# Optimization experiments

Hardware: AMD Instinct MI355X
Metric: run time of the kernel (lower is better)

## Reference

```python
import jax, jax.numpy as jnp
import numpy as np

N, E, F_IN, HID, H1, H2, H3, OUT = 10000, 160000, 50, 350, 4, 4, 6, 121


def _gat(x, src, dst, n, W, a_s, a_d, b, heads, C, concat):
    # PyG GATConv (dropout=0, eval): h = xW^T reshaped to [N,H,C]
    h = (x @ W.T).reshape(n, heads, C)
    alpha_src = jnp.einsum('nhc,hc->nh', h, a_s)  # [N,H]
    alpha_dst = jnp.einsum('nhc,hc->nh', h, a_d)  # [N,H]
    e = jax.nn.leaky_relu(alpha_src[src] + alpha_dst[dst], 0.2)  # [E,H]
    # numerically-stable segment softmax over incoming edges of each dst node
    m = jax.ops.segment_max(e, dst, num_segments=n)
    ee = jnp.exp(e - m[dst])
    s = jax.ops.segment_sum(ee, dst, num_segments=n)
    alpha = ee / s[dst]  # self-loops guarantee s > 0
    out = jax.ops.segment_sum(h[src] * alpha[:, :, None], dst, num_segments=n)  # [N,H,C]
    out = out.reshape(n, heads * C) if concat else out.mean(axis=1)
    return out + b


def setup_inputs() -> dict:
    key = jax.random.key(0)
    ks = jax.random.split(key, 16)
    sc = 0.05
    inp = {
        'x': jax.random.normal(ks[0], (N, F_IN), dtype=jnp.float32),
        'edge_index': jax.random.randint(ks[1], (2, E), 0, N, dtype=jnp.int64) if jax.config.jax_enable_x64 else jax.random.randint(ks[1], (2, E), 0, N, dtype=jnp.int32),
        'W1': jax.random.normal(ks[2], (H1 * HID, F_IN), dtype=jnp.float32) * sc,
        'a1s': jax.random.normal(ks[3], (H1, HID), dtype=jnp.float32) * sc,
        'a1d': jax.random.normal(ks[4], (H1, HID), dtype=jnp.float32) * sc,
        'b1': jnp.zeros((H1 * HID,), dtype=jnp.float32),
        'W2': jax.random.normal(ks[5], (H2 * HID, H1 * HID), dtype=jnp.float32) * sc,
        'a2s': jax.random.normal(ks[6], (H2, HID), dtype=jnp.float32) * sc,
        'a2d': jax.random.normal(ks[7], (H2, HID), dtype=jnp.float32) * sc,
        'b2': jnp.zeros((H2 * HID,), dtype=jnp.float32),
        'Wskip': jax.random.normal(ks[8], (H2 * HID, H1 * HID), dtype=jnp.float32) * sc,
        'W3': jax.random.normal(ks[9], (H3 * OUT, H2 * HID), dtype=jnp.float32) * sc,
        'a3s': jax.random.normal(ks[10], (H3, OUT), dtype=jnp.float32) * sc,
        'a3d': jax.random.normal(ks[11], (H3, OUT), dtype=jnp.float32) * sc,
        'b3': jnp.zeros((OUT,), dtype=jnp.float32),
    }
    return inp


def reference(x, edge_index, W1, a1s, a1d, b1, W2, a2s, a2d, b2, Wskip, W3, a3s, a3d, b3):
    n = x.shape[0]
    loops = jnp.arange(n, dtype=edge_index.dtype)  # PyG add_self_loops=True
    src = jnp.concatenate([edge_index[0], loops])
    dst = jnp.concatenate([edge_index[1], loops])
    h = jax.nn.elu(_gat(x, src, dst, n, W1, a1s, a1d, b1, H1, HID, True))
    x_in = h
    h = jax.nn.elu(_gat(h, src, dst, n, W2, a2s, a2d, b2, H2, HID, True))
    h = h + x_in @ Wskip.T  # skip connection (bias=False)
    return _gat(h, src, dst, n, W3, a3s, a3d, b3, H3, OUT, False)
```

## Files before the change

kernel.cpp:

```cpp
#include <hip/hip_runtime.h>
#include <math.h>

#define NNODES 10000
#define NEDGES 160000
#define E2 (NEDGES + NNODES)
#define F_IN 50
#define HIDC 350
#define NH1 4
#define NH2 4
#define NH3 6
#define OUTC 121
#define MAXE 96
#define KP1 64
#define KP2 1408
#define LD3 736
#define ROWSLACK 128

typedef __attribute__((ext_vector_type(8))) short short8;
typedef __attribute__((ext_vector_type(8))) unsigned short ushort8v;
typedef __attribute__((ext_vector_type(4))) float floatx4;

static __device__ __forceinline__ unsigned short f2bf(float f) {
    unsigned u = __float_as_uint(f);
    unsigned r = (u + 0x7fffu + ((u >> 16) & 1u)) >> 16;
    return (unsigned short)r;
}
static __device__ __forceinline__ float bf2f(unsigned short s) {
    return __uint_as_float(((unsigned)s) << 16);
}

#define GLL16(gp, lp)                                                      \
    __builtin_amdgcn_global_load_lds(                                      \
        (const __attribute__((address_space(1))) void*)(gp),               \
        (__attribute__((address_space(3))) void*)(lp), 16, 0, 0)

__global__ void count_kernel(const int* __restrict__ ei, int* __restrict__ cnt) {
    int i = blockIdx.x * blockDim.x + threadIdx.x;
    if (i >= E2) return;
    int dst = (i < NEDGES) ? ei[NEDGES + i] : (i - NEDGES);
    atomicAdd(&cnt[dst], 1);
}

__global__ void scan_kernel(const int* __restrict__ cnt, int* __restrict__ indptr,
                            int* __restrict__ cursor) {
    __shared__ int part[1024];
    int tid = threadIdx.x;
    const int CH = (NNODES + 1023) / 1024;
    int base = tid * CH;
    int s = 0;
    for (int i = 0; i < CH; i++) {
        int idx = base + i;
        if (idx < NNODES) s += cnt[idx];
    }
    part[tid] = s;
    __syncthreads();
    for (int off = 1; off < 1024; off <<= 1) {
        int v = (tid >= off) ? part[tid - off] : 0;
        __syncthreads();
        part[tid] += v;
        __syncthreads();
    }
    int run = (tid == 0) ? 0 : part[tid - 1];
    for (int i = 0; i < CH; i++) {
        int idx = base + i;
        if (idx < NNODES) {
            indptr[idx] = run;
            cursor[idx] = run;
            run += cnt[idx];
        }
    }
    if (tid == 0) indptr[NNODES] = part[1023];
}

__global__ void scatter_kernel(const int* __restrict__ ei, int* __restrict__ cursor,
                               int* __restrict__ esrc) {
    int i = blockIdx.x * blockDim.x + threadIdx.x;
    if (i >= E2) return;
    int src, dst;
    if (i < NEDGES) {
        src = ei[i];
        dst = ei[NEDGES + i];
    } else {
        src = dst = i - NEDGES;
    }
    int pos = atomicAdd(&cursor[dst], 1);
    esrc[pos] = src;
}

__global__ void splitW1_kernel(const float* __restrict__ W1,
                               unsigned short* __restrict__ w1Hi,
                               unsigned short* __restrict__ w1Lo) {
    int k = threadIdx.x;
    int r = blockIdx.x;
    float v = (k < F_IN) ? W1[(size_t)r * F_IN + k] : 0.f;
    unsigned short h = f2bf(v);
    w1Hi[(size_t)r * KP1 + k] = h;
    w1Lo[(size_t)r * KP1 + k] = f2bf(v - bf2f(h));
}

__global__ void splitB_kernel(const float* __restrict__ W2, const float* __restrict__ Wsk,
                              const float* __restrict__ W3,
                              unsigned short* __restrict__ w2Hi,
                              unsigned short* __restrict__ w3Hi) {
    int k = blockIdx.x * blockDim.x + threadIdx.x;
    if (k >= KP2) return;
    int r = blockIdx.y;
    const int K = 1400;
    const float* src;
    unsigned short* hi;
    int row;
    if (r < 1400) { src = W2; row = r; hi = w2Hi; }
    else if (r < 2800) { src = Wsk; row = r - 1400; hi = w2Hi + (size_t)1400 * KP2; }
    else { src = W3; row = r - 2800; hi = w3Hi; }
    float v = (k < K) ? src[(size_t)row * K + k] : 0.f;
    hi[(size_t)row * KP2 + k] = f2bf(v);
}

__global__ void atil_kernel(const float* __restrict__ W, const float* __restrict__ av_s,
                            const float* __restrict__ av_d, float* __restrict__ outS,
                            float* __restrict__ outD, int C, int K, int cchunk) {
    int k = blockIdx.x * 64 + (threadIdx.x & 63);
    if (k >= K) return;
    int h = blockIdx.y;
    int c0 = blockIdx.z * cchunk;
    int c1 = c0 + cchunk;
    if (c1 > C) c1 = C;
    float ss = 0.f, dd = 0.f;
    for (int c = c0; c < c1; c++) {
        float wv = W[((size_t)h * C + c) * K + k];
        ss = fmaf(wv, av_s[h * C + c], ss);
        dd = fmaf(wv, av_d[h * C + c], dd);
    }
    atomicAdd(&outS[(size_t)h * K + k], ss);
    atomicAdd(&outD[(size_t)h * K + k], dd);
}

__global__ void splitAT2_kernel(const float* __restrict__ atall,
                                unsigned short* __restrict__ atHi,
                                unsigned short* __restrict__ atLo) {
    int k = blockIdx.x * 64 + threadIdx.x;
    int r = blockIdx.y;
    float v = 0.f;
    if (k < 1400) {
        if (r < 4) v = atall[400 + r * 1400 + k];
        else if (r < 8) v = atall[6000 + (r - 4) * 1400 + k];
    }
    unsigned short h = f2bf(v);
    atHi[(size_t)r * KP2 + k] = h;
    atLo[(size_t)r * KP2 + k] = f2bf(v - bf2f(h));
}

__global__ __launch_bounds__(256) void alpha1x_kernel(const float* __restrict__ x,
                                                      const float* __restrict__ at1s,
                                                      const float* __restrict__ at1d,
                                                      float* __restrict__ as1,
                                                      float* __restrict__ ad1) {
    int wave = threadIdx.x >> 6, lane = threadIdx.x & 63;
    int n = blockIdx.x * 4 + wave;
    if (n >= NNODES) return;
    int kk = lane < F_IN ? lane : F_IN - 1;
    float v = (lane < F_IN) ? x[(size_t)n * F_IN + lane] : 0.f;
    float p[8];
#pragma unroll
    for (int h = 0; h < 4; h++) {
        p[h] = v * at1s[h * F_IN + kk];
        p[4 + h] = v * at1d[h * F_IN + kk];
    }
#pragma unroll
    for (int s = 0; s < 8; s++)
#pragma unroll
        for (int o = 32; o > 0; o >>= 1) p[s] += __shfl_xor(p[s], o, 64);
    if (lane == 0) {
#pragma unroll
        for (int h = 0; h < 4; h++) {
            as1[n * 4 + h] = p[h];
            ad1[n * 4 + h] = p[4 + h];
        }
    }
}

__global__ void zeropad_kernel(unsigned short* __restrict__ hi) {
    int i = blockIdx.x * 256 + threadIdx.x;
    if (i >= NNODES * 8) return;
    int n = i >> 3, c = 1400 + (i & 7);
    hi[(size_t)n * KP2 + c] = 0;
}

__global__ __launch_bounds__(256) void agg_x(
    const float* __restrict__ x, const float* __restrict__ as_n,
    const float* __restrict__ ad_n, const int* __restrict__ indptr,
    const int* __restrict__ esrc, unsigned short* __restrict__ xaggHi,
    unsigned short* __restrict__ xaggLo) {
    int n = blockIdx.x, tid = threadIdx.x;
    int s = indptr[n], e = indptr[n + 1];
    int deg = e - s;
    if (deg > MAXE) deg = MAXE;
    __shared__ int srcs[MAXE];
    __shared__ float wgt[MAXE * 4];

    if (tid < 64) {
        int lane = tid;
        float adv[4], mx[4], sm[4];
#pragma unroll
        for (int h = 0; h < 4; h++) {
            adv[h] = ad_n[n * 4 + h];
            mx[h] = -1e30f;
            sm[h] = 0.f;
        }
        for (int j = lane; j < deg; j += 64) {
            int sr = esrc[s + j];
            srcs[j] = sr;
#pragma unroll
            for (int h = 0; h < 4; h++) {
                float ev = as_n[sr * 4 + h] + adv[h];
                ev = ev > 0.f ? ev : 0.2f * ev;
                wgt[j * 4 + h] = ev;
                mx[h] = fmaxf(mx[h], ev);
            }
        }
#pragma unroll
        for (int h = 0; h < 4; h++)
#pragma unroll
            for (int o = 32; o > 0; o >>= 1) mx[h] = fmaxf(mx[h], __shfl_xor(mx[h], o, 64));
        for (int j = lane; j < deg; j += 64) {
#pragma unroll
            for (int h = 0; h < 4; h++) {
                float p = __expf(wgt[j * 4 + h] - mx[h]);
                wgt[j * 4 + h] = p;
                sm[h] += p;
            }
        }
#pragma unroll
        for (int h = 0; h < 4; h++) {
#pragma unroll
            for (int o = 32; o > 0; o >>= 1) sm[h] += __shfl_xor(sm[h], o, 64);
            sm[h] = 1.f / sm[h];
        }
        for (int j = lane; j < deg; j += 64) {
#pragma unroll
            for (int h = 0; h < 4; h++) wgt[j * 4 + h] *= sm[h];
        }
    }
    __syncthreads();

    int h = tid >> 6, k = tid & 63;
    float a = 0.f;
    if (k < F_IN) {
        float a2 = 0.f;
        int j = 0;
        for (; j + 1 < deg; j += 2) {
            a = fmaf(wgt[j * 4 + h], x[(size_t)srcs[j] * F_IN + k], a);
            a2 = fmaf(wgt[(j + 1) * 4 + h], x[(size_t)srcs[j + 1] * F_IN + k], a2);
        }
        if (j < deg) a = fmaf(wgt[j * 4 + h], x[(size_t)srcs[j] * F_IN + k], a);
        a += a2;
    }
    unsigned short hi = f2bf(a);
    xaggHi[(size_t)n * 256 + tid] = hi;
    xaggLo[(size_t)n * 256 + tid] = f2bf(a - bf2f(hi));
}

__global__ __launch_bounds__(256, 2) void gemm_h1(
    const unsigned short* __restrict__ xaggHi, const unsigned short* __restrict__ xaggLo,
    const unsigned short* __restrict__ w1Hi, const unsigned short* __restrict__ w1Lo,
    const float* __restrict__ bias, unsigned short* __restrict__ actHi) {
    __shared__ __align__(16) unsigned short sA[2][128 * 32];
    __shared__ __align__(16) unsigned short sB[2][256 * 32];
    int tid = threadIdx.x;
    int wave = tid >> 6, lane = tid & 63;
    int wm = (wave >> 1) * 64, wn = (wave & 1) * 128;
    int fr = lane & 15, kq = lane >> 4;
    int row0 = blockIdx.y * 128, col0 = blockIdx.x * 256;
    int hd = blockIdx.z;

    floatx4 acc[4][8];
#pragma unroll
    for (int i = 0; i < 4; i++)
#pragma unroll
        for (int j = 0; j < 8; j++)
#pragma unroll
            for (int q = 0; q < 4; q++) acc[i][j][q] = 0.f;

    int gpos = lane & 3;
    int rl = lane >> 2;
    int gsw = kq ^ ((fr >> 1) & 3);

    for (int k0 = 0; k0 < 64; k0 += 32) {
#pragma unroll
        for (int c = 0; c < 2; ++c) {
            int r = wave * 32 + c * 16 + rl;
            int g = gpos ^ ((r >> 1) & 3);
            size_t gofs = (size_t)(row0 + r) * 256 + hd * 64 + k0 + g * 8;
            size_t lofs = (size_t)r * 32 + (size_t)gpos * 8;
            GLL16(xaggHi + gofs, &sA[0][lofs]);
            GLL16(xaggLo + gofs, &sA[1][lofs]);
        }
#pragma unroll
        for (int c = 0; c < 4; ++c) {
            int r = wave * 64 + c * 16 + rl;
            int g = gpos ^ ((r >> 1) & 3);
            size_t gofs = (size_t)(hd * 350 + col0 + r) * KP1 + k0 + g * 8;
            size_t lofs = (size_t)r * 32 + (size_t)gpos * 8;
            GLL16(w1Hi + gofs, &sB[0][lofs]);
            GLL16(w1Lo + gofs, &sB[1][lofs]);
        }
        __syncthreads();

        short8 ah[4], al[4], bh[8], bl[8];
#pragma unroll
        for (int j = 0; j < 8; j++) {
            int rb = wn + j * 16 + fr;
            bh[j] = *(const short8*)&sB[0][rb * 32 + gsw * 8];
            bl[j] = *(const short8*)&sB[1][rb * 32 + gsw * 8];
        }
#pragma unroll
        for (int i = 0; i < 4; i++) {
            int ra = wm + i * 16 + fr;
            ah[i] = *(const short8*)&sA[0][ra * 32 + gsw * 8];
            al[i] = *(const short8*)&sA[1][ra * 32 + gsw * 8];
        }
#pragma unroll
        for (int i = 0; i < 4; i++)
#pragma unroll
            for (int j = 0; j < 8; j++) {
                acc[i][j] = __builtin_amdgcn_mfma_f32_16x16x32_bf16(ah[i], bh[j],
                                                                   acc[i][j], 0, 0, 0);
                acc[i][j] = __builtin_amdgcn_mfma_f32_16x16x32_bf16(al[i], bh[j],
                                                                   acc[i][j], 0, 0, 0);
                acc[i][j] = __builtin_amdgcn_mfma_f32_16x16x32_bf16(ah[i], bl[j],
                                                                   acc[i][j], 0, 0, 0);
            }
        __syncthreads();
    }

#pragma unroll
    for (int i = 0; i < 4; i++) {
#pragma unroll
        for (int rg = 0; rg < 4; rg++) {
            int rr = row0 + wm + i * 16 + kq * 4 + rg;
            if (rr >= NNODES) continue;
#pragma unroll
            for (int j = 0; j < 8; j++) {
                int cc = col0 + wn + j * 16 + fr;
                if (cc < 350) {
                    int gc = hd * 350 + cc;
                    float v = acc[i][j][rg] + bias[gc];
                    v = v > 0.f ? v : expm1f(v);
                    actHi[(size_t)rr * KP2 + gc] = f2bf(v);
                }
            }
        }
    }
}

__global__ __launch_bounds__(256) void alpha_mfma(
    const unsigned short* __restrict__ act, const unsigned short* __restrict__ tHi,
    const unsigned short* __restrict__ tLo, int H, float* __restrict__ asx,
    float* __restrict__ adx) {
    int wave = threadIdx.x >> 6, lane = threadIdx.x & 63;
    int row0 = (blockIdx.x * 4 + wave) * 16;
    if (row0 >= NNODES) return;
    int fr = lane & 15, kq = lane >> 4;
    floatx4 acc = {0.f, 0.f, 0.f, 0.f};
    const unsigned short* arow = act + (size_t)(row0 + fr) * KP2 + kq * 8;
    const unsigned short* brh = tHi + (size_t)fr * KP2 + kq * 8;
    const unsigned short* brl = tLo + (size_t)fr * KP2 + kq * 8;
#pragma unroll 4
    for (int k0 = 0; k0 < KP2; k0 += 32) {
        short8 a = *(const short8*)(arow + k0);
        short8 vh = *(const short8*)(brh + k0);
        short8 vl = *(const short8*)(brl + k0);
        acc = __builtin_amdgcn_mfma_f32_16x16x32_bf16(a, vh, acc, 0, 0, 0);
        acc = __builtin_amdgcn_mfma_f32_16x16x32_bf16(a, vl, acc, 0, 0, 0);
    }
#pragma unroll
    for (int rg = 0; rg < 4; rg++) {
        int rr = row0 + kq * 4 + rg;
        if (fr < H) asx[rr * H + fr] = acc[rg];
        else if (fr < 2 * H) adx[rr * H + (fr - H)] = acc[rg];
    }
}

template <int H>
__global__ __launch_bounds__(64) void alpha_edge(
    const float* __restrict__ as_n, const float* __restrict__ ad_n,
    const int* __restrict__ indptr, const int* __restrict__ esrc,
    float* __restrict__ walpha) {
    int n = blockIdx.x;
    int lane = threadIdx.x;
    int s = indptr[n], e = indptr[n + 1];
    int deg = e - s;
    if (deg > MAXE) deg = MAXE;
    __shared__ float wgt[MAXE * H];
    float adv[H], mx[H], sm[H];
#pragma unroll
    for (int h = 0; h < H; h++) {
        adv[h] = ad_n[n * H + h];
        mx[h] = -1e30f;
        sm[h] = 0.f;
    }
    for (int j = lane; j < deg; j += 64) {
        int sr = esrc[s + j];
#pragma unroll
        for (int h = 0; h < H; h++) {
            float ev = as_n[sr * H + h] + adv[h];
            ev = ev > 0.f ? ev : 0.2f * ev;
            wgt[j * H + h] = ev;
            mx[h] = fmaxf(mx[h], ev);
        }
    }
#pragma unroll
    for (int h = 0; h < H; h++)
#pragma unroll
        for (int o = 32; o > 0; o >>= 1) mx[h] = fmaxf(mx[h], __shfl_xor(mx[h], o, 64));
    for (int j = lane; j < deg; j += 64) {
#pragma unroll
        for (int h = 0; h < H; h++) {
            float p = __expf(wgt[j * H + h] - mx[h]);
            wgt[j * H + h] = p;
            sm[h] += p;
        }
    }
#pragma unroll
    for (int h = 0; h < H; h++) {
#pragma unroll
        for (int o = 32; o > 0; o >>= 1) sm[h] += __shfl_xor(sm[h], o, 64);
        sm[h] = 1.f / sm[h];
    }
    for (int j = lane; j < deg; j += 64) {
#pragma unroll
        for (int h = 0; h < H; h++) wgt[j * H + h] *= sm[h];
    }
    __syncthreads();
    for (int i = lane; i < deg * H; i += 64)
        walpha[(size_t)s * H + i] = wgt[i];
}

__global__ __launch_bounds__(256, 2) void gemm_b16(
    const unsigned short* __restrict__ A, const unsigned short* __restrict__ B,
    unsigned short* __restrict__ Cb, int NN, int M, int Kp, int ldc) {
    __shared__ __align__(16) unsigned short sA[128 * 32];
    __shared__ __align__(16) unsigned short sB[256 * 32];
    int tid = threadIdx.x;
    int wave = tid >> 6, lane = tid & 63;
    int wm = (wave >> 1) * 64, wn = (wave & 1) * 128;
    int fr = lane & 15, kq = lane >> 4;

    int gx = (int)gridDim.x;
    int nwg = gx * (int)gridDim.y;
    int bid = (int)blockIdx.y * gx + (int)blockIdx.x;
    int qq = nwg >> 3, rr8 = nwg & 7;
    int xcd = bid & 7, idx = bid >> 3;
    int nb = (xcd < rr8) ? xcd * (qq + 1) + idx : rr8 * (qq + 1) + (xcd - rr8) * qq + idx;
    int row0 = (nb / gx) * 128, col0 = (nb % gx) * 256;

    floatx4 acc[4][8];
#pragma unroll
    for (int i = 0; i < 4; i++)
#pragma unroll
        for (int j = 0; j < 8; j++)
#pragma unroll
            for (int q = 0; q < 4; q++) acc[i][j][q] = 0.f;

    int gpos = lane & 3;
    int rl = lane >> 2;
    int gsw = kq ^ ((fr >> 1) & 3);

    for (int k0 = 0; k0 < Kp; k0 += 32) {
#pragma unroll
        for (int c = 0; c < 2; ++c) {
            int r = wave * 32 + c * 16 + rl;
            int g = gpos ^ ((r >> 1) & 3);
            GLL16(A + (size_t)(row0 + r) * Kp + k0 + g * 8,
                  &sA[(size_t)r * 32 + (size_t)gpos * 8]);
        }
#pragma unroll
        for (int c = 0; c < 4; ++c) {
            int r = wave * 64 + c * 16 + rl;
            int g = gpos ^ ((r >> 1) & 3);
            GLL16(B + (size_t)(col0 + r) * Kp + k0 + g * 8,
                  &sB[(size_t)r * 32 + (size_t)gpos * 8]);
        }
        __syncthreads();

        short8 ah[4], bh[8];
#pragma unroll
        for (int j = 0; j < 8; j++) {
            int rb = wn + j * 16 + fr;
            bh[j] = *(const short8*)&sB[rb * 32 + gsw * 8];
        }
#pragma unroll
        for (int i = 0; i < 4; i++) {
            int ra = wm + i * 16 + fr;
            ah[i] = *(const short8*)&sA[ra * 32 + gsw * 8];
        }
#pragma unroll
        for (int i = 0; i < 4; i++)
#pragma unroll
            for (int j = 0; j < 8; j++)
                acc[i][j] = __builtin_amdgcn_mfma_f32_16x16x32_bf16(ah[i], bh[j],
                                                                   acc[i][j], 0, 0, 0);
        __syncthreads();
    }

#pragma unroll
    for (int i = 0; i < 4; i++) {
#pragma unroll
        for (int rg = 0; rg < 4; rg++) {
            int rrow = row0 + wm + i * 16 + kq * 4 + rg;
            if (rrow >= NN) continue;
#pragma unroll
            for (int j = 0; j < 8; j++) {
                int cc = col0 + wn + j * 16 + fr;
                if (cc < M) Cb[(size_t)rrow * ldc + cc] = f2bf(acc[i][j][rg]);
            }
        }
    }
}

#define AGG_T 192
__global__ __launch_bounds__(AGG_T) void agg2(
    const unsigned short* __restrict__ hpreb, int ldh,
    const int* __restrict__ indptr, const int* __restrict__ esrc,
    const float* __restrict__ walpha, const float* __restrict__ bias,
    unsigned short* __restrict__ outHi, int Kp,
    const float* __restrict__ atns, const float* __restrict__ atnd,
    float* __restrict__ asx, float* __restrict__ adx) {
    constexpr int H = 4, C = 350, HC = 1400, HN = 6;
    int n = blockIdx.x;
    int tid = threadIdx.x;
    int s = indptr[n], e = indptr[n + 1];
    int deg = e - s;
    if (deg > MAXE) deg = MAXE;

    __shared__ int srcs[MAXE];
    __shared__ float wgt[MAXE * H];
    __shared__ float sAl[16];
    if (tid < 16) sAl[tid] = 0.f;
    for (int i = tid; i < deg; i += AGG_T) srcs[i] = esrc[s + i];
    for (int i = tid; i < deg * H; i += AGG_T) wgt[i] = walpha[(size_t)s * H + i];
    __syncthreads();

    constexpr int NV8 = HC / 8;
    float p[2 * HN];
#pragma unroll
    for (int q = 0; q < 2 * HN; q++) p[q] = 0.f;

    for (int c8 = tid; c8 < NV8; c8 += AGG_T) {
        int cb = c8 * 8;
        int h0 = cb / C;
        int sp = (h0 + 1) * C - cb;
        if (sp > 8) sp = 8;
        int h1 = (h0 + 1 < H) ? h0 + 1 : h0;
        float av[8];
#pragma unroll
        for (int q = 0; q < 8; q++) av[q] = 0.f;
        int j = 0;
        for (; j + 7 < deg; j += 8) {
            ushort8v v[8];
            float w0[8], w1[8];
#pragma unroll
            for (int t = 0; t < 8; t++)
                v[t] = *(const ushort8v*)(hpreb + (size_t)srcs[j + t] * ldh + cb);
#pragma unroll
            for (int t = 0; t < 8; t++) {
                w0[t] = wgt[(j + t) * H + h0];
                w1[t] = wgt[(j + t) * H + h1];
            }
#pragma unroll
            for (int t = 0; t < 8; t++)
#pragma unroll
                for (int q = 0; q < 8; q++)
                    av[q] = fmaf(q < sp ? w0[t] : w1[t], bf2f(v[t][q]), av[q]);
        }
        for (; j + 3 < deg; j += 4) {
            ushort8v v[4];
            float w0[4], w1[4];
#pragma unroll
            for (int t = 0; t < 4; t++)
                v[t] = *(const ushort8v*)(hpreb + (size_t)srcs[j + t] * ldh + cb);
#pragma unroll
            for (int t = 0; t < 4; t++) {
                w0[t] = wgt[(j + t) * H + h0];
                w1[t] = wgt[(j + t) * H + h1];
            }
#pragma unroll
            for (int t = 0; t < 4; t++)
#pragma unroll
                for (int q = 0; q < 8; q++)
                    av[q] = fmaf(q < sp ? w0[t] : w1[t], bf2f(v[t][q]), av[q]);
        }
        for (; j < deg; j++) {
            const ushort8v v0 = *(const ushort8v*)(hpreb + (size_t)srcs[j] * ldh + cb);
            float wa0 = wgt[j * H + h0], wa1 = wgt[j * H + h1];
#pragma unroll
            for (int q = 0; q < 8; q++) av[q] = fmaf(q < sp ? wa0 : wa1, bf2f(v0[q]), av[q]);
        }
#pragma unroll
        for (int q = 0; q < 8; q++) av[q] += bias[cb + q];
#pragma unroll
        for (int q = 0; q < 8; q++) av[q] = av[q] > 0.f ? av[q] : expm1f(av[q]);
        const ushort8v sk = *(const ushort8v*)(hpreb + (size_t)n * ldh + 1400 + cb);
#pragma unroll
        for (int q = 0; q < 8; q++) av[q] += bf2f(sk[q]);
#pragma unroll
        for (int h = 0; h < HN; h++) {
            float ss = 0.f, dd = 0.f;
#pragma unroll
            for (int q = 0; q < 8; q++) {
                ss = fmaf(av[q], atns[(size_t)h * HC + cb + q], ss);
                dd = fmaf(av[q], atnd[(size_t)h * HC + cb + q], dd);
            }
            p[h] += ss;
            p[HN + h] += dd;
        }
        ushort8v hi8;
#pragma unroll
        for (int q = 0; q < 8; q++) hi8[q] = f2bf(av[q]);
        *(ushort8v*)(outHi + (size_t)n * Kp + cb) = hi8;
    }
    for (int c = HC + tid; c < Kp; c += AGG_T) outHi[(size_t)n * Kp + c] = 0;
#pragma unroll
    for (int q = 0; q < 2 * HN; q++)
#pragma unroll
        for (int o = 32; o > 0; o >>= 1) p[q] += __shfl_xor(p[q], o, 64);
    if ((tid & 63) == 0) {
#pragma unroll
        for (int q = 0; q < 2 * HN; q++) atomicAdd(&sAl[q], p[q]);
    }
    __syncthreads();
    if (tid < HN) asx[n * HN + tid] = sAl[tid];
    else if (tid < 2 * HN) adx[n * HN + (tid - HN)] = sAl[tid];
}

template <int H, int C>
__global__ __launch_bounds__(AGG_T) void agg3(
    const unsigned short* __restrict__ hpreb, int ldh,
    const int* __restrict__ indptr, const int* __restrict__ esrc,
    const float* __restrict__ walpha, const float* __restrict__ bias,
    float* __restrict__ outF) {
    constexpr int HC = H * C;
    int n = blockIdx.x;
    int tid = threadIdx.x;
    int s = indptr[n], e = indptr[n + 1];
    int deg = e - s;
    if (deg > MAXE) deg = MAXE;

    __shared__ int srcs[MAXE];
    __shared__ float wgt[MAXE * H];
    __shared__ float aggsh[HC];
    for (int i = tid; i < deg; i += AGG_T) srcs[i] = esrc[s + i];
    for (int i = tid; i < deg * H; i += AGG_T) wgt[i] = walpha[(size_t)s * H + i];
    __syncthreads();

    constexpr int NV8 = (HC + 7) / 8;
    for (int c8 = tid; c8 < NV8; c8 += AGG_T) {
        int cb = c8 * 8;
        int h0 = cb / C;
        if (h0 >= H) h0 = H - 1;
        int sp = (h0 + 1) * C - cb;
        if (sp > 8) sp = 8;
        int h1 = (h0 + 1 < H) ? h0 + 1 : h0;
        float av[8];
#pragma unroll
        for (int q = 0; q < 8; q++) av[q] = 0.f;
        int j = 0;
        for (; j + 7 < deg; j += 8) {
            ushort8v v[8];
            float w0[8], w1[8];
#pragma unroll
            for (int t = 0; t < 8; t++)
                v[t] = *(const ushort8v*)(hpreb + (size_t)srcs[j + t] * ldh + cb);
#pragma unroll
            for (int t = 0; t < 8; t++) {
                w0[t] = wgt[(j + t) * H + h0];
                w1[t] = wgt[(j + t) * H + h1];
            }
#pragma unroll
            for (int t = 0; t < 8; t++)
#pragma unroll
                for (int q = 0; q < 8; q++)
                    av[q] = fmaf(q < sp ? w0[t] : w1[t], bf2f(v[t][q]), av[q]);
        }
        for (; j + 3 < deg; j += 4) {
            ushort8v v[4];
            float w0[4], w1[4];
#pragma unroll
            for (int t = 0; t < 4; t++)
                v[t] = *(const ushort8v*)(hpreb + (size_t)srcs[j + t] * ldh + cb);
#pragma unroll
            for (int t = 0; t < 4; t++) {
                w0[t] = wgt[(j + t) * H + h0];
                w1[t] = wgt[(j + t) * H + h1];
            }
#pragma unroll
            for (int t = 0; t < 4; t++)
#pragma unroll
                for (int q = 0; q < 8; q++)
                    av[q] = fmaf(q < sp ? w0[t] : w1[t], bf2f(v[t][q]), av[q]);
        }
        for (; j < deg; j++) {
            const ushort8v v0 = *(const ushort8v*)(hpreb + (size_t)srcs[j] * ldh + cb);
            float wa0 = wgt[j * H + h0], wa1 = wgt[j * H + h1];
#pragma unroll
            for (int q = 0; q < 8; q++) av[q] = fmaf(q < sp ? wa0 : wa1, bf2f(v0[q]), av[q]);
        }
#pragma unroll
        for (int q = 0; q < 8; q++)
            if (cb + q < HC) aggsh[cb + q] = av[q];
    }
    __syncthreads();
    for (int c = tid; c < C; c += AGG_T) {
        float sres = 0.f;
#pragma unroll
        for (int h = 0; h < H; h++) sres += aggsh[h * C + c];
        outF[(size_t)n * C + c] = sres * (1.f / (float)H) + bias[c];
    }
}

extern "C" void kernel_launch(void* const* d_in, const int* in_sizes, int n_in,
                              void* d_out, int out_size, void* d_ws, size_t ws_size,
                              hipStream_t stream) {
    const float* x = (const float*)d_in[0];
    const int* ei = (const int*)d_in[1];
    const float* W1 = (const float*)d_in[2];
    const float* a1s = (const float*)d_in[3];
    const float* a1d = (const float*)d_in[4];
    const float* b1 = (const float*)d_in[5];
    const float* W2 = (const float*)d_in[6];
    const float* a2s = (const float*)d_in[7];
    const float* a2d = (const float*)d_in[8];
    const float* b2 = (const float*)d_in[9];
    const float* Wsk = (const float*)d_in[10];
    const float* W3 = (const float*)d_in[11];
    const float* a3s = (const float*)d_in[12];
    const float* a3d = (const float*)d_in[13];
    const float* b3 = (const float*)d_in[14];
    float* out = (float*)d_out;

    char* w = (char*)d_ws;
    size_t off = 0;
    auto alloc = [&](size_t bytes) -> char* {
        char* p = w + off;
        off += (bytes + 255) & ~(size_t)255;
        return p;
    };
    unsigned short* hpreb = (unsigned short*)alloc((size_t)(NNODES + ROWSLACK) * 2800 * 2);
    unsigned short* actHi = (unsigned short*)alloc((size_t)(NNODES + ROWSLACK) * KP2 * 2);
    unsigned short* xaggHi = (unsigned short*)alloc((size_t)(NNODES + ROWSLACK) * 256 * 2);
    unsigned short* xaggLo = (unsigned short*)alloc((size_t)(NNODES + ROWSLACK) * 256 * 2);
    unsigned short* w1Hi = (unsigned short*)alloc((size_t)(1400 + 512) * KP1 * 2);
    unsigned short* w1Lo = (unsigned short*)alloc((size_t)(1400 + 512) * KP1 * 2);
    unsigned short* w2Hi = (unsigned short*)alloc((size_t)(2800 + ROWSLACK) * KP2 * 2);
    unsigned short* w3Hi = (unsigned short*)alloc((size_t)(726 + ROWSLACK) * KP2 * 2);
    unsigned short* at2Hi = (unsigned short*)alloc((size_t)16 * KP2 * 2);
    unsigned short* at2Lo = (unsigned short*)alloc((size_t)16 * KP2 * 2);
    float* atall = (float*)alloc((size_t)28400 * 4);
    int* cnt = (int*)alloc((size_t)(NNODES + 16) * 4);
    float* at1s = atall;
    float* at1d = atall + 200;
    float* at2s = atall + 400;
    float* at2d = atall + 6000;
    float* at3s = atall + 11600;
    float* at3d = atall + 20000;
    float* asP = (float*)alloc((size_t)NNODES * 6 * 4);
    float* adP = (float*)alloc((size_t)NNODES * 6 * 4);
    float* asQ = (float*)alloc((size_t)NNODES * 6 * 4);
    float* adQ = (float*)alloc((size_t)NNODES * 6 * 4);
    int* indptr = (int*)alloc((size_t)(NNODES + 16) * 4);
    int* cursor = (int*)alloc((size_t)(NNODES + 16) * 4);
    int* esrc = (int*)alloc((size_t)E2 * 4);
    float* walpha = (float*)alloc((size_t)E2 * 6 * 4);

    size_t zbytes = (size_t)((char*)cnt - (char*)atall) + (NNODES + 16) * 4;
    hipMemsetAsync(atall, 0, zbytes, stream);

    splitW1_kernel<<<1400, 64, 0, stream>>>(W1, w1Hi, w1Lo);
    splitB_kernel<<<dim3(6, 2800 + 726), 256, 0, stream>>>(W2, Wsk, W3, w2Hi, w3Hi);
    atil_kernel<<<dim3(1, 4, 5), 64, 0, stream>>>(W1, a1s, a1d, at1s, at1d, HIDC, F_IN, 70);
    atil_kernel<<<dim3(22, 4, 5), 64, 0, stream>>>(W2, a2s, a2d, at2s, at2d, HIDC, 1400, 70);
    atil_kernel<<<dim3(22, 6, 4), 64, 0, stream>>>(W3, a3s, a3d, at3s, at3d, OUTC, 1400, 31);
    splitAT2_kernel<<<dim3(22, 16), 64, 0, stream>>>(atall, at2Hi, at2Lo);
    alpha1x_kernel<<<(NNODES + 3) / 4, 256, 0, stream>>>(x, at1s, at1d, asP, adP);

    count_kernel<<<(E2 + 255) / 256, 256, 0, stream>>>(ei, cnt);
    scan_kernel<<<1, 1024, 0, stream>>>(cnt, indptr, cursor);
    scatter_kernel<<<(E2 + 255) / 256, 256, 0, stream>>>(ei, cursor, esrc);

    zeropad_kernel<<<(NNODES * 8 + 255) / 256, 256, 0, stream>>>(actHi);

    dim3 blk(256);
    int gy = (NNODES + 127) / 128;

    agg_x<<<NNODES, 256, 0, stream>>>(x, asP, adP, indptr, esrc, xaggHi, xaggLo);
    gemm_h1<<<dim3(2, gy, 4), blk, 0, stream>>>(xaggHi, xaggLo, w1Hi, w1Lo, b1, actHi);
    alpha_mfma<<<(NNODES / 16 + 3) / 4, 256, 0, stream>>>(actHi, at2Hi, at2Lo, 4, asQ, adQ);
    alpha_edge<4><<<NNODES, 64, 0, stream>>>(asQ, adQ, indptr, esrc, walpha);

    {
        int M = 2800;
        dim3 grid((M + 255) / 256, gy);
        gemm_b16<<<grid, blk, 0, stream>>>(actHi, w2Hi, hpreb, NNODES, M, KP2, 2800);
        agg2<<<NNODES, AGG_T, 0, stream>>>(hpreb, 2800, indptr, esrc, walpha, b2,
                                           actHi, KP2, at3s, at3d, asP, adP);
    }
    {
        alpha_edge<6><<<NNODES, 64, 0, stream>>>(asP, adP, indptr, esrc, walpha);
        int M = NH3 * OUTC;
        dim3 grid((M + 255) / 256, gy);
        gemm_b16<<<grid, blk, 0, stream>>>(actHi, w3Hi, hpreb, NNODES, M, KP2, LD3);
        agg3<NH3, OUTC><<<NNODES, AGG_T, 0, stream>>>(
            hpreb, LD3, indptr, esrc, walpha, b3, out);
    }
}
```

Measured before the change: 619.5 us.

## Add 256x256 eight-wave double-buffered GEMM for layer-2 projection

Replaces the 128x256 four-wave bf16 GEMM for the layer-2 projection with a new 512-thread kernel using 256x256 tiles. It double-buffers A and B in LDS and interleaves global-to-LDS loads with MFMA phases, using explicit barriers, waitcnt and setprio. The aim is to hide load latency and improve data reuse per tile. It uses more LDS and registers, and the activation buffer is padded so the taller row tiles can read past the last node.

```diff
diff --git a/kernel.cpp b/kernel.cpp
--- a/kernel.cpp
+++ b/kernel.cpp
@@ -436,6 +436,131 @@
         walpha[(size_t)s * H + i] = wgt[i];
 }
 
+#define PH_MFMA(CH)                                                          \
+    __builtin_amdgcn_s_barrier();                                            \
+    asm volatile("s_waitcnt lgkmcnt(0)" ::: "memory");                       \
+    __builtin_amdgcn_sched_barrier(0);                                       \
+    __builtin_amdgcn_s_setprio(1);                                           \
+    _Pragma("unroll")                                                        \
+    for (int rf = 0; rf < 4; rf++) {                                         \
+        _Pragma("unroll")                                                    \
+        for (int cf = 0; cf < 4; cf++)                                       \
+            acc[(CH) * 4 + rf][cf] = __builtin_amdgcn_mfma_f32_16x16x32_bf16( \
+                a[rf], bfr[cf], acc[(CH) * 4 + rf][cf], 0, 0, 0);            \
+    }                                                                        \
+    __builtin_amdgcn_s_setprio(0);
+
+__global__ __launch_bounds__(512, 2) void gemm_8p(
+    const unsigned short* __restrict__ A, const unsigned short* __restrict__ B,
+    unsigned short* __restrict__ Cb, int NN, int M, int Kp, int ldc) {
+    __shared__ __align__(16) unsigned short sA[2][256 * 32];
+    __shared__ __align__(16) unsigned short sB[2][256 * 32];
+    int tid = threadIdx.x;
+    int w = tid >> 6, lane = tid & 63;
+    int wr = w >> 2, wc = w & 3;
+    int fr = lane & 15, kq = lane >> 4;
+
+    int gx = (int)gridDim.x;
+    int nwg = gx * (int)gridDim.y;
+    int bid = (int)blockIdx.y * gx + (int)blockIdx.x;
+    int qq = nwg >> 3, rr8 = nwg & 7;
+    int xcd = bid & 7, bdx = bid >> 3;
+    int nb = (xcd < rr8) ? xcd * (qq + 1) + bdx : rr8 * (qq + 1) + (xcd - rr8) * qq + bdx;
+    int row0 = (nb / gx) * 256, col0 = (nb % gx) * 256;
+
+    floatx4 acc[8][4];
+#pragma unroll
+    for (int i = 0; i < 8; i++)
+#pragma unroll
+        for (int j = 0; j < 4; j++)
+#pragma unroll
+            for (int q = 0; q < 4; q++) acc[i][j][q] = 0.f;
+
+    auto stage = [&](unsigned short* plane, const unsigned short* g, int rbase,
+                     int kofs) {
+#pragma unroll
+        for (int l = 0; l < 2; l++) {
+            int ix = l * 512 + tid, row = ix >> 2, sl = ix & 3, gp = sl ^ (row & 3);
+            GLL16(g + (size_t)(rbase + row) * Kp + kofs + gp * 8,
+                  plane + (size_t)row * 32 + sl * 8);
+        }
+    };
+    auto rdA = [&](const unsigned short* plane, int ch, short8* a) {
+#pragma unroll
+        for (int rf = 0; rf < 4; rf++) {
+            int row = wr * 128 + ch * 64 + rf * 16 + fr;
+            a[rf] = *(const short8*)(plane + (size_t)row * 32 + (kq ^ (row & 3)) * 8);
+        }
+    };
+    auto rdB = [&](const unsigned short* plane, short8* b) {
+#pragma unroll
+        for (int cf = 0; cf < 4; cf++) {
+            int row = wc * 64 + cf * 16 + fr;
+            b[cf] = *(const short8*)(plane + (size_t)row * 32 + (kq ^ (row & 3)) * 8);
+        }
+    };
+
+    const int nkt = Kp >> 6;
+    stage(sA[0], A, row0, 0);
+    stage(sB[0], B, col0, 0);
+    stage(sB[1], B, col0, 32);
+    asm volatile("s_waitcnt vmcnt(2)" ::: "memory");
+    __builtin_amdgcn_sched_barrier(0);
+    __builtin_amdgcn_s_barrier();
+
+    short8 a[4], bfr[4];
+    for (int t = 0; t < nkt; ++t) {
+        int kt = t << 6;
+        bool more = (t + 1 < nkt);
+        rdA(sA[0], 0, a);
+        rdB(sB[0], bfr);
+        PH_MFMA(0)
+        stage(sA[1], A, row0, kt + 32);
+        __builtin_amdgcn_s_barrier();
+        rdA(sA[0], 1, a);
+        PH_MFMA(1)
+        if (more) {
+            stage(sB[0], B, col0, kt + 64);
+            asm volatile("s_waitcnt vmcnt(2)" ::: "memory");
+        } else {
+            asm volatile("s_waitcnt vmcnt(0)" ::: "memory");
+        }
+        __builtin_amdgcn_sched_barrier(0);
+        __builtin_amdgcn_s_barrier();
+        rdA(sA[1], 0, a);
+        rdB(sB[1], bfr);
+        PH_MFMA(0)
+        if (more) stage(sA[0], A, row0, kt + 64);
+        __builtin_amdgcn_s_barrier();
+        rdA(sA[1], 1, a);
+        PH_MFMA(1)
+        if (more) {
+            stage(sB[1], B, col0, kt + 96);
+            asm volatile("s_waitcnt vmcnt(2)" ::: "memory");
+            __builtin_amdgcn_sched_barrier(0);
+        }
+        __builtin_amdgcn_s_barrier();
+    }
+
+#pragma unroll
+    for (int ch = 0; ch < 2; ch++) {
+#pragma unroll
+        for (int rf = 0; rf < 4; rf++) {
+#pragma unroll
+            for (int rg = 0; rg < 4; rg++) {
+                int rrow = row0 + wr * 128 + ch * 64 + rf * 16 + kq * 4 + rg;
+                if (rrow >= NN) continue;
+#pragma unroll
+                for (int cf = 0; cf < 4; cf++) {
+                    int cc = col0 + wc * 64 + cf * 16 + fr;
+                    if (cc < M)
+                        Cb[(size_t)rrow * ldc + cc] = f2bf(acc[ch * 4 + rf][cf][rg]);
+                }
+            }
+        }
+    }
+}
+
 __global__ __launch_bounds__(256, 2) void gemm_b16(
     const unsigned short* __restrict__ A, const unsigned short* __restrict__ B,
     unsigned short* __restrict__ Cb, int NN, int M, int Kp, int ldc) {
@@ -746,7 +871,7 @@
         return p;
     };
     unsigned short* hpreb = (unsigned short*)alloc((size_t)(NNODES + ROWSLACK) * 2800 * 2);
-    unsigned short* actHi = (unsigned short*)alloc((size_t)(NNODES + ROWSLACK) * KP2 * 2);
+    unsigned short* actHi = (unsigned short*)alloc((size_t)(NNODES + 384) * KP2 * 2);
     unsigned short* xaggHi = (unsigned short*)alloc((size_t)(NNODES + ROWSLACK) * 256 * 2);
     unsigned short* xaggLo = (unsigned short*)alloc((size_t)(NNODES + ROWSLACK) * 256 * 2);
     unsigned short* w1Hi = (unsigned short*)alloc((size_t)(1400 + 512) * KP1 * 2);
@@ -799,8 +924,8 @@
 
     {
         int M = 2800;
-        dim3 grid((M + 255) / 256, gy);
-        gemm_b16<<<grid, blk, 0, stream>>>(actHi, w2Hi, hpreb, NNODES, M, KP2, 2800);
+        dim3 grid((M + 255) / 256, (NNODES + 255) / 256);
+        gemm_8p<<<grid, 512, 0, stream>>>(actHi, w2Hi, hpreb, NNODES, M, KP2, 2800);
         agg2<<<NNODES, AGG_T, 0, stream>>>(hpreb, 2800, indptr, esrc, walpha, b2,
                                            actHi, KP2, at3s, at3d, asP, adP);
     }
```

Result: no change. 617.0 us (-0.4%).
